# Kernel optimization log

Hardware: AMD Instinct MI355X
Metric: run time of the kernel (lower is better)

## Reference

```python
import jax, jax.numpy as jnp
import numpy as np

BN_EPS = 1e-5
LRELU_SLOPE = 0.2


def setup_inputs() -> dict:
    key = jax.random.key(0)
    ks = jax.random.split(key, 5)
    B, C1, M, C2, N, C_out = 8, 256, 4096, 128, 16384, 256
    feature = jax.random.normal(ks[0], (B, C1, M), dtype=jnp.float32)
    encoder_feature = jax.random.normal(ks[1], (B, C2, N), dtype=jnp.float32)
    interp_index = jax.random.randint(ks[2], (B, N, 1), 0, M, dtype=jnp.int64)
    # ConvTranspose1d(384, 256, 1) weight has shape [in, out, 1] -> store as [in, out]
    W = jax.random.normal(ks[3], (C1 + C2, C_out), dtype=jnp.float32) * 0.05
    b = jax.random.normal(ks[4], (C_out,), dtype=jnp.float32) * 0.05
    gamma = jnp.ones((C_out,), dtype=jnp.float32)
    beta = jnp.zeros((C_out,), dtype=jnp.float32)
    return {"feature": feature, "encoder_feature": encoder_feature,
            "interp_index": interp_index, "W": W, "b": b,
            "gamma": gamma, "beta": beta}


def reference(feature, encoder_feature, interp_index, W, b, gamma, beta):
    # feature: [B, C1, M], encoder_feature: [B, C2, N], interp_index: [B, N, 1]
    idx = interp_index[..., 0]                                  # [B, N]
    # index_points on feature.permute(0,2,1) then permute back == gather along last dim
    interp_feature = jnp.take_along_axis(feature, idx[:, None, :], axis=2)  # [B, C1, N]
    x = jnp.concatenate([encoder_feature, interp_feature], axis=1)          # [B, C1+C2, N]
    # ConvTranspose1d(kernel=1): y[b,o,n] = sum_i x[b,i,n] * W[i,o] + b[o]
    y = jnp.einsum('bin,io->bon', x, W) + b[None, :, None]      # [B, C_out, N]
    # BatchNorm1d (training mode: batch stats over (B, N), biased variance)
    mean = jnp.mean(y, axis=(0, 2), keepdims=True)
    var = jnp.mean(jnp.square(y - mean), axis=(0, 2), keepdims=True)
    y = (y - mean) * jax.lax.rsqrt(var + BN_EPS)
    y = y * gamma[None, :, None] + beta[None, :, None]
    # LeakyReLU(0.2)
    return jnp.where(y > 0, y, LRELU_SLOPE * y)
```

## Files before the change

kernel.cpp:

```cpp
#include <hip/hip_runtime.h>
#include <hip/hip_bf16.h>

#define C1    256
#define C2    128
#define COUT  256
#define KTOT  384
#define MM    4096
#define NN    16384
#define BB    8
#define BN_EPS 1e-5f
#define SLOPE 0.2f

typedef float  f32x4  __attribute__((ext_vector_type(4)));
typedef __bf16 bf16x8 __attribute__((ext_vector_type(8)));
typedef unsigned short u16x8 __attribute__((ext_vector_type(8)));
typedef unsigned short u16x4 __attribute__((ext_vector_type(4)));

#define GLOBAL_AS __attribute__((address_space(1)))
#define LDS_AS    __attribute__((address_space(3)))

static __device__ __forceinline__ unsigned short f2bf(float f) {
    unsigned int u = __builtin_bit_cast(unsigned int, f);
    unsigned int r = (u + 0x7FFFu + ((u >> 16) & 1u)) >> 16;
    return (unsigned short)r;
}

static __device__ __forceinline__ float bf2f(unsigned short b) {
    return __builtin_bit_cast(float, (unsigned int)b << 16);
}

static __device__ __forceinline__ bf16x8 ld_frag_g(const unsigned short* p) {
    union { u16x8 s; bf16x8 b; } cvt;
    cvt.s = *reinterpret_cast<const u16x8*>(p);
    return cvt.b;
}

__global__ __launch_bounds__(256) void k0_transpose(const float* __restrict__ in,
                                                    unsigned short* __restrict__ out,
                                                    int R, int C) {
    __shared__ float f[64][68];
    const int c0 = blockIdx.x * 64, r0 = blockIdx.y * 64;
    const float* inb = in + (size_t)blockIdx.z * R * C;
    unsigned short* outb = out + (size_t)blockIdx.z * R * C;
    const int t = threadIdx.x;
#pragma unroll
    for (int q = 0; q < 4; q++) {
        int idx = q * 256 + t;
        int ri = idx >> 4, c4 = (idx & 15) * 4;
        float4 v = *reinterpret_cast<const float4*>(&inb[(size_t)(r0 + ri) * C + c0 + c4]);
        *reinterpret_cast<float4*>(&f[ri][c4]) = v;
    }
    __syncthreads();
#pragma unroll
    for (int q = 0; q < 4; q++) {
        int idx = q * 256 + t;
        int oc = idx >> 4, rq = (idx & 15) * 4;
        u16x4 u;
#pragma unroll
        for (int j = 0; j < 4; j++) u[j] = f2bf(f[rq + j][oc]);
        *reinterpret_cast<u16x4*>(&outb[(size_t)(c0 + oc) * R + r0 + rq]) = u;
    }
}

__global__ __launch_bounds__(256, 4) void k1_zt(const unsigned short* __restrict__ featT,
                                                const unsigned short* __restrict__ Wt,
                                                unsigned short* __restrict__ ZtB) {
    const int mb = blockIdx.x * 64, ob = blockIdx.y * 64, b = blockIdx.z;
    const int tid = threadIdx.x;
    const int wid = tid >> 6, lane = tid & 63;
    const int r = lane & 15, g = lane >> 4;
    const int wm = (wid >> 1) * 32, wo = (wid & 1) * 32;

    f32x4 acc[2][2];
#pragma unroll
    for (int i = 0; i < 2; i++)
#pragma unroll
        for (int j = 0; j < 2; j++) acc[i][j] = (f32x4){0.f, 0.f, 0.f, 0.f};

    const unsigned short* fA = featT + (size_t)(b * MM + mb) * C1;

#pragma unroll
    for (int kp = 0; kp < 2; kp++)
#pragma unroll
        for (int ks = 0; ks < 4; ks++) {
            const int kb = kp * 128 + ks * 32 + g * 8;
            bf16x8 a0 = ld_frag_g(&fA[(size_t)(wm +  0 + r) * C1 + kb]);
            bf16x8 a1 = ld_frag_g(&fA[(size_t)(wm + 16 + r) * C1 + kb]);
            bf16x8 b0 = ld_frag_g(&Wt[(size_t)(ob + wo +  0 + r) * KTOT + C2 + kb]);
            bf16x8 b1 = ld_frag_g(&Wt[(size_t)(ob + wo + 16 + r) * KTOT + C2 + kb]);
            acc[0][0] = __builtin_amdgcn_mfma_f32_16x16x32_bf16(a0, b0, acc[0][0], 0, 0, 0);
            acc[0][1] = __builtin_amdgcn_mfma_f32_16x16x32_bf16(a0, b1, acc[0][1], 0, 0, 0);
            acc[1][0] = __builtin_amdgcn_mfma_f32_16x16x32_bf16(a1, b0, acc[1][0], 0, 0, 0);
            acc[1][1] = __builtin_amdgcn_mfma_f32_16x16x32_bf16(a1, b1, acc[1][1], 0, 0, 0);
        }

#pragma unroll
    for (int fm = 0; fm < 2; fm++)
#pragma unroll
        for (int fo = 0; fo < 2; fo++)
#pragma unroll
            for (int i = 0; i < 4; i++) {
                int m = mb + wm + fm * 16 + g * 4 + i;
                int o = ob + wo + fo * 16 + r;
                ZtB[(size_t)(b * MM + m) * COUT + o] = f2bf(acc[fm][fo][i]);
            }
}

__global__ __launch_bounds__(256, 4) void k2_main(const unsigned short* __restrict__ encT,
                                                  const unsigned short* __restrict__ Wt,
                                                  const float* __restrict__ bias,
                                                  const int*   __restrict__ idx,
                                                  const unsigned short* __restrict__ ZtB,
                                                  float* __restrict__ y,
                                                  float* __restrict__ sums,
                                                  float* __restrict__ sumsq) {
    const int nb = blockIdx.x * 128, ob = blockIdx.y * 64, b = blockIdx.z;
    const int tid = threadIdx.x;

    __shared__ unsigned short ZlB[128 * 64];
    __shared__ float lsum[64], lsq[64];
    if (tid < 64) { lsum[tid] = 0.f; lsq[tid] = 0.f; }

    const int wid = tid >> 6, lane = tid & 63;
    const int r = lane & 15, g = lane >> 4;
    const int wo = (wid >> 1) * 32;
    const int wn = (wid & 1) * 64;

    {
        const int* idxb = idx + b * NN + nb;
        const int lrow = lane >> 3, lcol = lane & 7;
#pragma unroll
        for (int it = 0; it < 4; it++) {
            const int wrow = wid * 32 + it * 8;
            const int row  = wrow + lrow;
            const int zi   = idxb[row];
            const unsigned short* src = &ZtB[(size_t)(b * MM + zi) * COUT + ob +
                                             ((lcol ^ (row & 7)) << 3)];
            __builtin_amdgcn_global_load_lds(
                (const GLOBAL_AS unsigned int*)src,
                (LDS_AS unsigned int*)(&ZlB[wrow * 64]), 16, 0, 0);
        }
    }

    bf16x8 wf[4][2];
#pragma unroll
    for (int ks = 0; ks < 4; ks++)
#pragma unroll
        for (int fr = 0; fr < 2; fr++)
            wf[ks][fr] = ld_frag_g(&Wt[(size_t)(ob + wo + fr * 16 + r) * KTOT +
                                       ks * 32 + g * 8]);

    f32x4 acc[2][4];
#pragma unroll
    for (int i = 0; i < 2; i++)
#pragma unroll
        for (int j = 0; j < 4; j++) acc[i][j] = (f32x4){0.f, 0.f, 0.f, 0.f};

    const unsigned short* eB = encT + (size_t)(b * NN + nb) * C2;
#pragma unroll
    for (int ks = 0; ks < 4; ks++) {
        const int kb = ks * 32 + g * 8;
        bf16x8 bfr[4];
#pragma unroll
        for (int fn = 0; fn < 4; fn++)
            bfr[fn] = ld_frag_g(&eB[(size_t)(wn + fn * 16 + r) * C2 + kb]);
#pragma unroll
        for (int fn = 0; fn < 4; fn++) {
            acc[0][fn] = __builtin_amdgcn_mfma_f32_16x16x32_bf16(wf[ks][0], bfr[fn], acc[0][fn], 0, 0, 0);
            acc[1][fn] = __builtin_amdgcn_mfma_f32_16x16x32_bf16(wf[ks][1], bfr[fn], acc[1][fn], 0, 0, 0);
        }
    }

    __syncthreads();

    float bi[2][4];
#pragma unroll
    for (int fo = 0; fo < 2; fo++)
#pragma unroll
        for (int i = 0; i < 4; i++)
            bi[fo][i] = bias[ob + wo + fo * 16 + g * 4 + i];

    float s_[2][4] = {{0.f,0.f,0.f,0.f},{0.f,0.f,0.f,0.f}};
    float q_[2][4] = {{0.f,0.f,0.f,0.f},{0.f,0.f,0.f,0.f}};
#pragma unroll
    for (int fo = 0; fo < 2; fo++)
#pragma unroll
        for (int fn = 0; fn < 4; fn++) {
            const int n_loc = wn + fn * 16 + r;
            const int obase = wo + fo * 16 + g * 4;
            const int pg = (obase >> 3) ^ (n_loc & 7);
            const int h  = (obase >> 2) & 1;
            const u16x4 z = *reinterpret_cast<const u16x4*>(
                &ZlB[n_loc * 64 + (pg << 3) + (h << 2)]);
#pragma unroll
            for (int i = 0; i < 4; i++) {
                int o_loc = obase + i;
                float v = acc[fo][fn][i] + bf2f(z[i]) + bi[fo][i];
                y[(size_t)(b * COUT + ob + o_loc) * NN + nb + n_loc] = v;
                s_[fo][i] += v;
                q_[fo][i] += v * v;
            }
        }

#pragma unroll
    for (int d = 1; d < 16; d <<= 1)
#pragma unroll
        for (int fo = 0; fo < 2; fo++)
#pragma unroll
            for (int i = 0; i < 4; i++) {
                s_[fo][i] += __shfl_xor(s_[fo][i], d);
                q_[fo][i] += __shfl_xor(q_[fo][i], d);
            }
    if (r == 0) {
#pragma unroll
        for (int fo = 0; fo < 2; fo++)
#pragma unroll
            for (int i = 0; i < 4; i++) {
                int o_loc = wo + fo * 16 + g * 4 + i;
                atomicAdd(&lsum[o_loc], s_[fo][i]);
                atomicAdd(&lsq[o_loc],  q_[fo][i]);
            }
    }
    __syncthreads();
    if (tid < 64) {
        atomicAdd(&sums [b * COUT + ob + tid], lsum[tid]);
        atomicAdd(&sumsq[b * COUT + ob + tid], lsq[tid]);
    }
}

__global__ void k3_stats(const float* __restrict__ sums,
                         const float* __restrict__ sumsq,
                         const float* __restrict__ gamma,
                         const float* __restrict__ beta,
                         float* __restrict__ ac) {
    const int o = threadIdx.x;
    float s = 0.f, q = 0.f;
#pragma unroll
    for (int b = 0; b < BB; b++) {
        s += sums [b * COUT + o];
        q += sumsq[b * COUT + o];
    }
    const float inv_cnt = 1.0f / ((float)BB * (float)NN);
    float mean = s * inv_cnt;
    float var  = q * inv_cnt - mean * mean;
    float a = gamma[o] * rsqrtf(var + BN_EPS);
    float c = beta[o] - mean * a;
    ac[o] = a;
    ac[COUT + o] = c;
}

__global__ __launch_bounds__(256) void k4_norm(float* __restrict__ y,
                                               const float* __restrict__ ac) {
    const size_t total4 = (size_t)BB * COUT * NN / 4;
    const size_t stride = (size_t)gridDim.x * 256;
    for (size_t i = (size_t)blockIdx.x * 256 + threadIdx.x; i < total4; i += stride) {
        float4 v = reinterpret_cast<float4*>(y)[i];
        int o = (int)((i * 4) >> 14) & 255;
        float a = ac[o], c = ac[COUT + o];
        float t0 = a * v.x + c; v.x = t0 > 0.f ? t0 : SLOPE * t0;
        float t1 = a * v.y + c; v.y = t1 > 0.f ? t1 : SLOPE * t1;
        float t2 = a * v.z + c; v.z = t2 > 0.f ? t2 : SLOPE * t2;
        float t3 = a * v.w + c; v.w = t3 > 0.f ? t3 : SLOPE * t3;
        reinterpret_cast<float4*>(y)[i] = v;
    }
}

extern "C" void kernel_launch(void* const* d_in, const int* in_sizes, int n_in,
                              void* d_out, int out_size, void* d_ws, size_t ws_size,
                              hipStream_t stream) {
    const float* feature = (const float*)d_in[0];
    const float* enc     = (const float*)d_in[1];
    const int*   idx     = (const int*)  d_in[2];
    const float* W       = (const float*)d_in[3];
    const float* bias    = (const float*)d_in[4];
    const float* gamma   = (const float*)d_in[5];
    const float* beta    = (const float*)d_in[6];
    float* out = (float*)d_out;

    float* sums  = (float*)d_ws;
    float* sumsq = sums + BB * COUT;
    float* ac    = sumsq + BB * COUT;
    unsigned short* ZtB   = (unsigned short*)(ac + 2 * COUT);
    unsigned short* featT = ZtB   + (size_t)BB * MM * COUT;
    unsigned short* encT  = featT + (size_t)BB * MM * C1;
    unsigned short* Wt    = encT  + (size_t)BB * NN * C2;

    hipMemsetAsync(sums, 0, 2 * BB * COUT * sizeof(float), stream);

    k0_transpose<<<dim3(MM / 64, C1 / 64, BB),   256, 0, stream>>>(feature, featT, C1, MM);
    k0_transpose<<<dim3(NN / 64, C2 / 64, BB),   256, 0, stream>>>(enc, encT, C2, NN);
    k0_transpose<<<dim3(COUT / 64, KTOT / 64, 1),256, 0, stream>>>(W, Wt, KTOT, COUT);

    k1_zt  <<<dim3(MM / 64, COUT / 64, BB), 256, 0, stream>>>(featT, Wt, ZtB);
    k2_main<<<dim3(NN / 128, COUT / 64, BB), 256, 0, stream>>>(encT, Wt, bias, idx, ZtB,
                                                               out, sums, sumsq);
    k3_stats<<<1, COUT, 0, stream>>>(sums, sumsq, gamma, beta, ac);
    k4_norm<<<2048, 256, 0, stream>>>(out, ac);
}
```

Before: 346.9 us.

## Recompute GEMM in second pass to fuse BatchNorm and LeakyReLU into output write

Splits the main kernel into a stats-only pass that no longer stores the pre-normalization output, and a final pass that recomputes the small GEMM plus gathered Z term. The final pass computes per-channel scale and shift from the accumulated sums and writes the normalized, activated result directly. This removes the full fp32 intermediate write and the separate normalize kernel's read-modify-write of the large output. In exchange, the GEMM and the gather from Z are done twice.

After: 358.0 us. 1.03x slower.

```diff
diff --git a/kernel.cpp b/kernel.cpp
--- a/kernel.cpp
+++ b/kernel.cpp
@@ -106,14 +106,13 @@
             }
 }
 
-__global__ __launch_bounds__(256, 4) void k2_main(const unsigned short* __restrict__ encT,
-                                                  const unsigned short* __restrict__ Wt,
-                                                  const float* __restrict__ bias,
-                                                  const int*   __restrict__ idx,
-                                                  const unsigned short* __restrict__ ZtB,
-                                                  float* __restrict__ y,
-                                                  float* __restrict__ sums,
-                                                  float* __restrict__ sumsq) {
+__global__ __launch_bounds__(256, 4) void k2_stats(const unsigned short* __restrict__ encT,
+                                                   const unsigned short* __restrict__ Wt,
+                                                   const float* __restrict__ bias,
+                                                   const int*   __restrict__ idx,
+                                                   const unsigned short* __restrict__ ZtB,
+                                                   float* __restrict__ sums,
+                                                   float* __restrict__ sumsq) {
     const int nb = blockIdx.x * 128, ob = blockIdx.y * 64, b = blockIdx.z;
     const int tid = threadIdx.x;
 
@@ -194,9 +193,7 @@
                 &ZlB[n_loc * 64 + (pg << 3) + (h << 2)]);
 #pragma unroll
             for (int i = 0; i < 4; i++) {
-                int o_loc = obase + i;
                 float v = acc[fo][fn][i] + bf2f(z[i]) + bi[fo][i];
-                y[(size_t)(b * COUT + ob + o_loc) * NN + nb + n_loc] = v;
                 s_[fo][i] += v;
                 q_[fo][i] += v * v;
             }
@@ -228,41 +225,119 @@
     }
 }
 
-__global__ void k3_stats(const float* __restrict__ sums,
-                         const float* __restrict__ sumsq,
-                         const float* __restrict__ gamma,
-                         const float* __restrict__ beta,
-                         float* __restrict__ ac) {
-    const int o = threadIdx.x;
-    float s = 0.f, q = 0.f;
-#pragma unroll
-    for (int b = 0; b < BB; b++) {
-        s += sums [b * COUT + o];
-        q += sumsq[b * COUT + o];
-    }
-    const float inv_cnt = 1.0f / ((float)BB * (float)NN);
-    float mean = s * inv_cnt;
-    float var  = q * inv_cnt - mean * mean;
-    float a = gamma[o] * rsqrtf(var + BN_EPS);
-    float c = beta[o] - mean * a;
-    ac[o] = a;
-    ac[COUT + o] = c;
-}
-
-__global__ __launch_bounds__(256) void k4_norm(float* __restrict__ y,
-                                               const float* __restrict__ ac) {
-    const size_t total4 = (size_t)BB * COUT * NN / 4;
-    const size_t stride = (size_t)gridDim.x * 256;
-    for (size_t i = (size_t)blockIdx.x * 256 + threadIdx.x; i < total4; i += stride) {
-        float4 v = reinterpret_cast<float4*>(y)[i];
-        int o = (int)((i * 4) >> 14) & 255;
-        float a = ac[o], c = ac[COUT + o];
-        float t0 = a * v.x + c; v.x = t0 > 0.f ? t0 : SLOPE * t0;
-        float t1 = a * v.y + c; v.y = t1 > 0.f ? t1 : SLOPE * t1;
-        float t2 = a * v.z + c; v.z = t2 > 0.f ? t2 : SLOPE * t2;
-        float t3 = a * v.w + c; v.w = t3 > 0.f ? t3 : SLOPE * t3;
-        reinterpret_cast<float4*>(y)[i] = v;
-    }
+__global__ __launch_bounds__(256, 4) void k2_final(const unsigned short* __restrict__ encT,
+                                                   const unsigned short* __restrict__ Wt,
+                                                   const float* __restrict__ bias,
+                                                   const int*   __restrict__ idx,
+                                                   const unsigned short* __restrict__ ZtB,
+                                                   const float* __restrict__ sums,
+                                                   const float* __restrict__ sumsq,
+                                                   const float* __restrict__ gamma,
+                                                   const float* __restrict__ beta,
+                                                   float* __restrict__ y) {
+    const int nb = blockIdx.x * 128, ob = blockIdx.y * 64, b = blockIdx.z;
+    const int tid = threadIdx.x;
+
+    __shared__ unsigned short ZlB[128 * 64];
+    __shared__ float la[64], lc[64];
+
+    const int wid = tid >> 6, lane = tid & 63;
+    const int r = lane & 15, g = lane >> 4;
+    const int wo = (wid >> 1) * 32;
+    const int wn = (wid & 1) * 64;
+
+    {
+        const int* idxb = idx + b * NN + nb;
+        const int lrow = lane >> 3, lcol = lane & 7;
+#pragma unroll
+        for (int it = 0; it < 4; it++) {
+            const int wrow = wid * 32 + it * 8;
+            const int row  = wrow + lrow;
+            const int zi   = idxb[row];
+            const unsigned short* src = &ZtB[(size_t)(b * MM + zi) * COUT + ob +
+                                             ((lcol ^ (row & 7)) << 3)];
+            __builtin_amdgcn_global_load_lds(
+                (const GLOBAL_AS unsigned int*)src,
+                (LDS_AS unsigned int*)(&ZlB[wrow * 64]), 16, 0, 0);
+        }
+    }
+
+    if (tid < 64) {
+        const int o = ob + tid;
+        float s = 0.f, q = 0.f;
+#pragma unroll
+        for (int bb = 0; bb < BB; bb++) {
+            s += sums [bb * COUT + o];
+            q += sumsq[bb * COUT + o];
+        }
+        const float inv_cnt = 1.0f / ((float)BB * (float)NN);
+        float mean = s * inv_cnt;
+        float var  = q * inv_cnt - mean * mean;
+        float a = gamma[o] * rsqrtf(var + BN_EPS);
+        la[tid] = a;
+        lc[tid] = beta[o] - mean * a;
+    }
+
+    bf16x8 wf[4][2];
+#pragma unroll
+    for (int ks = 0; ks < 4; ks++)
+#pragma unroll
+        for (int fr = 0; fr < 2; fr++)
+            wf[ks][fr] = ld_frag_g(&Wt[(size_t)(ob + wo + fr * 16 + r) * KTOT +
+                                       ks * 32 + g * 8]);
+
+    f32x4 acc[2][4];
+#pragma unroll
+    for (int i = 0; i < 2; i++)
+#pragma unroll
+        for (int j = 0; j < 4; j++) acc[i][j] = (f32x4){0.f, 0.f, 0.f, 0.f};
+
+    const unsigned short* eB = encT + (size_t)(b * NN + nb) * C2;
+#pragma unroll
+    for (int ks = 0; ks < 4; ks++) {
+        const int kb = ks * 32 + g * 8;
+        bf16x8 bfr[4];
+#pragma unroll
+        for (int fn = 0; fn < 4; fn++)
+            bfr[fn] = ld_frag_g(&eB[(size_t)(wn + fn * 16 + r) * C2 + kb]);
+#pragma unroll
+        for (int fn = 0; fn < 4; fn++) {
+            acc[0][fn] = __builtin_amdgcn_mfma_f32_16x16x32_bf16(wf[ks][0], bfr[fn], acc[0][fn], 0, 0, 0);
+            acc[1][fn] = __builtin_amdgcn_mfma_f32_16x16x32_bf16(wf[ks][1], bfr[fn], acc[1][fn], 0, 0, 0);
+        }
+    }
+
+    __syncthreads();
+
+    float bi[2][4], af[2][4], cf[2][4];
+#pragma unroll
+    for (int fo = 0; fo < 2; fo++)
+#pragma unroll
+        for (int i = 0; i < 4; i++) {
+            int ol = wo + fo * 16 + g * 4 + i;
+            bi[fo][i] = bias[ob + ol];
+            af[fo][i] = la[ol];
+            cf[fo][i] = lc[ol];
+        }
+
+#pragma unroll
+    for (int fo = 0; fo < 2; fo++)
+#pragma unroll
+        for (int fn = 0; fn < 4; fn++) {
+            const int n_loc = wn + fn * 16 + r;
+            const int obase = wo + fo * 16 + g * 4;
+            const int pg = (obase >> 3) ^ (n_loc & 7);
+            const int h  = (obase >> 2) & 1;
+            const u16x4 z = *reinterpret_cast<const u16x4*>(
+                &ZlB[n_loc * 64 + (pg << 3) + (h << 2)]);
+#pragma unroll
+            for (int i = 0; i < 4; i++) {
+                float v = acc[fo][fn][i] + bf2f(z[i]) + bi[fo][i];
+                float t = af[fo][i] * v + cf[fo][i];
+                t = t > 0.f ? t : SLOPE * t;
+                y[(size_t)(b * COUT + ob + obase + i) * NN + nb + n_loc] = t;
+            }
+        }
 }
 
 extern "C" void kernel_launch(void* const* d_in, const int* in_sizes, int n_in,
@@ -279,8 +354,7 @@
 
     float* sums  = (float*)d_ws;
     float* sumsq = sums + BB * COUT;
-    float* ac    = sumsq + BB * COUT;
-    unsigned short* ZtB   = (unsigned short*)(ac + 2 * COUT);
+    unsigned short* ZtB   = (unsigned short*)(sumsq + BB * COUT);
     unsigned short* featT = ZtB   + (size_t)BB * MM * COUT;
     unsigned short* encT  = featT + (size_t)BB * MM * C1;
     unsigned short* Wt    = encT  + (size_t)BB * NN * C2;
@@ -291,9 +365,9 @@
     k0_transpose<<<dim3(NN / 64, C2 / 64, BB),   256, 0, stream>>>(enc, encT, C2, NN);
     k0_transpose<<<dim3(COUT / 64, KTOT / 64, 1),256, 0, stream>>>(W, Wt, KTOT, COUT);
 
-    k1_zt  <<<dim3(MM / 64, COUT / 64, BB), 256, 0, stream>>>(featT, Wt, ZtB);
-    k2_main<<<dim3(NN / 128, COUT / 64, BB), 256, 0, stream>>>(encT, Wt, bias, idx, ZtB,
-                                                               out, sums, sumsq);
-    k3_stats<<<1, COUT, 0, stream>>>(sums, sumsq, gamma, beta, ac);
-    k4_norm<<<2048, 256, 0, stream>>>(out, ac);
-}
+    k1_zt   <<<dim3(MM / 64, COUT / 64, BB), 256, 0, stream>>>(featT, Wt, ZtB);
+    k2_stats<<<dim3(NN / 128, COUT / 64, BB), 256, 0, stream>>>(encT, Wt, bias, idx, ZtB,
+                                                                sums, sumsq);
+    k2_final<<<dim3(NN / 128, COUT / 64, BB), 256, 0, stream>>>(encT, Wt, bias, idx, ZtB,
+                                                                sums, sumsq, gamma, beta, out);
+}
```
